# Performance work log

Measured on AMD Instinct MI355X. Metric: run time of the kernel, lower is better.

## Reference

```python
import jax, jax.numpy as jnp
import numpy as np

B, S, D_IN, D_OUT = 4, 2048, 4096, 4096


def setup_inputs() -> dict:
    key = jax.random.key(0)
    k1, k2, k3 = jax.random.split(key, 3)
    # int32 activations (already quantized upstream in the original pipeline)
    x_i32 = jax.random.randint(k1, (B, S, D_IN), -128, 128, dtype=jnp.int32)
    # int8 weights in [in, out] layout (Linear weight transposed), symmetric range [-127, 127]
    weight_i8 = jax.random.randint(k2, (D_IN, D_OUT), -127, 128, dtype=jnp.int32).astype(jnp.int8)
    # bias quantized affine to int32 (scale=16 in original)
    bias_i32 = jax.random.randint(k3, (D_OUT,), -2048, 2048, dtype=jnp.int32)
    return {"x_i32": x_i32, "weight_i8": weight_i8, "bias_i32": bias_i32, "out_shift": 7}


def reference(x_i32, weight_i8, bias_i32, out_shift):
    x_shape = x_i32.shape
    x2d = x_i32.reshape(-1, x_shape[-1]).astype(jnp.int32)  # [tokens, d_in]
    # int8 weights upcast to int32, plain int32 matmul with int32 accumulation
    y = jnp.matmul(x2d, weight_i8.astype(jnp.int32), preferred_element_type=jnp.int32)
    y = y + bias_i32  # fused bias add (int32)
    if out_shift > 0:  # out_shift is a static Python int
        y = jnp.right_shift(y, out_shift)  # arithmetic shift on signed int32
    return y.reshape(*x_shape[:-1], y.shape[-1]).astype(jnp.int32)
```

## Files before the change

kernel.cpp:

```cpp
#include <hip/hip_runtime.h>

using int32x4 = __attribute__((ext_vector_type(4))) int;

#define BM 256
#define BN 256
#define TBUF 32768

__global__ __launch_bounds__(256) void pack_x_kernel(const int32x4* __restrict__ x,
                                                     int32x4* __restrict__ xp,
                                                     int nvec) {
    int t = blockIdx.x * 256 + threadIdx.x;
    if (t >= nvec) return;
    int32x4 a = x[t * 4 + 0];
    int32x4 b = x[t * 4 + 1];
    int32x4 c = x[t * 4 + 2];
    int32x4 d = x[t * 4 + 3];
    int32x4 o;
    o.x = (a.x & 255) | ((a.y & 255) << 8) | ((a.z & 255) << 16) | (a.w << 24);
    o.y = (b.x & 255) | ((b.y & 255) << 8) | ((b.z & 255) << 16) | (b.w << 24);
    o.z = (c.x & 255) | ((c.y & 255) << 8) | ((c.z & 255) << 16) | (c.w << 24);
    o.w = (d.x & 255) | ((d.y & 255) << 8) | ((d.z & 255) << 16) | (d.w << 24);
    xp[t] = o;
}

__global__ __launch_bounds__(256) void transform_w_kernel(const int* __restrict__ w,
                                                          unsigned char* __restrict__ wt,
                                                          int K, int N) {
    __shared__ unsigned char tileT[64][72];
    int tx = threadIdx.x & 15;
    int ty = threadIdx.x >> 4;
    int n0 = blockIdx.x * 64;
    int k0 = blockIdx.y * 64;
#pragma unroll
    for (int r = 0; r < 4; ++r) {
        int row = ty * 4 + r;
        int32x4 v = *(const int32x4*)&w[(size_t)(k0 + row) * N + n0 + tx * 4];
        tileT[tx * 4 + 0][row] = (unsigned char)(v.x & 255);
        tileT[tx * 4 + 1][row] = (unsigned char)(v.y & 255);
        tileT[tx * 4 + 2][row] = (unsigned char)(v.z & 255);
        tileT[tx * 4 + 3][row] = (unsigned char)(v.w & 255);
    }
    __syncthreads();
#pragma unroll
    for (int r = 0; r < 4; ++r) {
        int row = ty * 4 + r;
        uchar4 v = *(const uchar4*)&tileT[row][tx * 4];
        *(uchar4*)&wt[(size_t)(n0 + row) * K + k0 + tx * 4] = v;
    }
}

__global__ __launch_bounds__(512, 2) void gemm_i8_deep(
    const char* __restrict__ A,
    const char* __restrict__ Bt,
    const int* __restrict__ bias,
    const int* __restrict__ shiftp,
    int* __restrict__ C,
    int M, int N, int K) {
    __shared__ char smem[4 * TBUF];

    const int nbn = N / BN;
    const int nwg = gridDim.x;
    const int bid = blockIdx.x;
    const int cpx = nwg >> 3;
    const int swz = (bid & 7) * cpx + (bid >> 3);
    const int m0 = (swz / nbn) * BM;
    const int n0 = (swz % nbn) * BN;

    const int t = threadIdx.x;
    const int lane = t & 63;
    const int wave = t >> 6;
    const int wr = wave >> 2;
    const int wc = wave & 3;

    const int s_row = t >> 2;
    const int s_col = ((t & 3) << 4) ^ (((t >> 3) & 3) << 4);
    const char* a_src = A + (size_t)(m0 + s_row) * K + s_col;
    const char* b_src = Bt + (size_t)(n0 + s_row) * K + s_col;
    const size_t jstr = (size_t)128 * K;
    char* lds_st = smem + t * 16;

    const int lr = lane & 15;
    const int lc = (lane >> 4) << 4;
    const int xr = ((lr >> 1) & 3) << 4;
    const int a_off = ((wr << 7) + lr) * 64 + (lc ^ xr);
    const int b_off = 16384 + ((wc << 6) + lr) * 64 + (lc ^ xr);

    int32x4 acc[8][4] = {};

    const int nt = K / 64;

#define GLL(src, dst)                                                 \
    __builtin_amdgcn_global_load_lds(                                 \
        (const __attribute__((address_space(1))) void*)(src),        \
        (__attribute__((address_space(3))) void*)(dst), 16, 0, 0)

#define FENCE asm volatile("" ::: "memory")
#define BARR                           \
    do {                               \
        FENCE;                         \
        __builtin_amdgcn_s_barrier();  \
        FENCE;                         \
    } while (0)
#define LGKM0                                                   \
    do {                                                        \
        asm volatile("s_waitcnt lgkmcnt(0)" ::: "memory");      \
        __builtin_amdgcn_sched_barrier(0);                      \
    } while (0)
#define VMW(n)                                                  \
    do {                                                        \
        asm volatile("s_waitcnt vmcnt(" #n ")" ::: "memory");   \
        __builtin_amdgcn_sched_barrier(0);                      \
    } while (0)

#define TILE(TT, DOSTAGE, VMWSTMT)                                                     \
    do {                                                                               \
        const int base_ = ((TT) & 3) * TBUF;                                           \
        const int sb_ = (((TT) + 3) & 3) * TBUF;                                       \
        const size_t kc_ = (size_t)((TT) + 3) * 64;                                    \
        int32x4 af[4], bf[4];                                                          \
        _Pragma("unroll") for (int i = 0; i < 4; ++i)                                  \
            af[i] = *(const int32x4*)&smem[base_ + a_off + i * 1024];                  \
        _Pragma("unroll") for (int i = 0; i < 4; ++i)                                  \
            bf[i] = *(const int32x4*)&smem[base_ + b_off + i * 1024];                  \
        if (DOSTAGE) {                                                                 \
            GLL(a_src + kc_, lds_st + sb_);                                            \
            GLL(a_src + jstr + kc_, lds_st + sb_ + 8192);                              \
        }                                                                              \
        BARR;                                                                          \
        LGKM0;                                                                         \
        __builtin_amdgcn_s_setprio(1);                                                 \
        _Pragma("unroll") for (int i = 0; i < 4; ++i)                                  \
            _Pragma("unroll") for (int j = 0; j < 4; ++j)                              \
                acc[i][j] =                                                            \
                    __builtin_amdgcn_mfma_i32_16x16x64_i8(af[i], bf[j], acc[i][j], 0, 0, 0); \
        __builtin_amdgcn_s_setprio(0);                                                 \
        BARR;                                                                          \
        _Pragma("unroll") for (int i = 0; i < 4; ++i)                                  \
            af[i] = *(const int32x4*)&smem[base_ + a_off + (4 + i) * 1024];            \
        if (DOSTAGE) {                                                                 \
            GLL(b_src + kc_, lds_st + sb_ + 16384);                                    \
            GLL(b_src + jstr + kc_, lds_st + sb_ + 16384 + 8192);                      \
        }                                                                              \
        BARR;                                                                          \
        LGKM0;                                                                         \
        __builtin_amdgcn_s_setprio(1);                                                 \
        _Pragma("unroll") for (int i = 0; i < 4; ++i)                                  \
            _Pragma("unroll") for (int j = 0; j < 4; ++j)                              \
                acc[4 + i][j] =                                                        \
                    __builtin_amdgcn_mfma_i32_16x16x64_i8(af[i], bf[j], acc[4 + i][j], 0, 0, 0); \
        __builtin_amdgcn_s_setprio(0);                                                 \
        VMWSTMT;                                                                       \
        BARR;                                                                          \
    } while (0)

#pragma unroll
    for (int p = 0; p < 3; ++p) {
        GLL(a_src + p * 64, lds_st + p * TBUF);
        GLL(a_src + jstr + p * 64, lds_st + p * TBUF + 8192);
        GLL(b_src + p * 64, lds_st + p * TBUF + 16384);
        GLL(b_src + jstr + p * 64, lds_st + p * TBUF + 24576);
    }
    VMW(8);
    BARR;

    int tt = 0;
    for (; tt < nt - 3; ++tt) TILE(tt, 1, VMW(8));
    TILE(tt, 0, VMW(4)); ++tt;
    TILE(tt, 0, VMW(0)); ++tt;
    TILE(tt, 0, (void)0);

    const int s = *shiftp;
    const int crow = (lane >> 4) << 2;
    const int ccol = lane & 15;
    int bv[4];
#pragma unroll
    for (int nf = 0; nf < 4; ++nf) bv[nf] = bias[n0 + wc * 64 + nf * 16 + ccol];
#pragma unroll
    for (int mf = 0; mf < 8; ++mf) {
        const int grow0 = m0 + wr * 128 + mf * 16 + crow;
#pragma unroll
        for (int nf = 0; nf < 4; ++nf) {
            const int gcol = n0 + wc * 64 + nf * 16 + ccol;
#pragma unroll
            for (int r = 0; r < 4; ++r) {
                int y = acc[mf][nf][r] + bv[nf];
                y = (s > 0) ? (y >> s) : y;
                C[(size_t)(grow0 + r) * N + gcol] = y;
            }
        }
    }
#undef GLL
#undef FENCE
#undef BARR
#undef LGKM0
#undef VMW
#undef TILE
}

extern "C" void kernel_launch(void* const* d_in, const int* in_sizes, int n_in,
                              void* d_out, int out_size, void* d_ws, size_t ws_size,
                              hipStream_t stream) {
    const int* x = (const int*)d_in[0];
    const int* w = (const int*)d_in[1];
    const int* bias = (const int*)d_in[2];
    const int* shiftp = (const int*)d_in[3];
    int* out = (int*)d_out;

    const int N = in_sizes[2];
    const int K = in_sizes[1] / N;
    const int M = in_sizes[0] / K;

    char* xp = (char*)d_ws;
    unsigned char* wt = (unsigned char*)d_ws + (size_t)M * K;

    int nvec = (int)(((long long)M * K) / 16);
    pack_x_kernel<<<(nvec + 255) / 256, 256, 0, stream>>>((const int32x4*)x, (int32x4*)xp, nvec);

    dim3 tgrid(N / 64, K / 64);
    transform_w_kernel<<<tgrid, 256, 0, stream>>>(w, wt, K, N);

    int nwg = (M / BM) * (N / BN);
    gemm_i8_deep<<<nwg, 512, 0, stream>>>(xp, (const char*)wt, bias, shiftp, out, M, N, K);
}
```

Before: 188.8 us.

## Switch to 32x32x32 int8 MFMA with register double-buffered fragment pipeline

Replaces the 16x16x64 int8 MFMA tiling with 32x32x32 MFMAs, giving 4x2 accumulator blocks per wave. LDS fragment reads are split into two halves (X and Y). The next tile's first half is prefetched into registers while the current tile's MFMAs run. This drops from four barriers per K-tile to one, meant to cut synchronisation stalls and overlap LDS latency with compute. The prologue now waits for all initial loads and issues a redundant B load that is later overwritten. The epilogue is rewritten for the 32x32 accumulator layout, which adds room for subtle ordering or layout bugs.

New measurement: 208.6 us. 1.11x slower.

```diff
diff --git a/kernel.cpp b/kernel.cpp
--- a/kernel.cpp
+++ b/kernel.cpp
@@ -1,6 +1,7 @@
 #include <hip/hip_runtime.h>
 
 using int32x4 = __attribute__((ext_vector_type(4))) int;
+using int32x16 = __attribute__((ext_vector_type(16))) int;
 
 #define BM 256
 #define BN 256
@@ -49,7 +50,7 @@
     }
 }
 
-__global__ __launch_bounds__(512, 2) void gemm_i8_deep(
+__global__ __launch_bounds__(512, 2) void gemm_i8_pipe(
     const char* __restrict__ A,
     const char* __restrict__ Bt,
     const int* __restrict__ bias,
@@ -79,13 +80,16 @@
     const size_t jstr = (size_t)128 * K;
     char* lds_st = smem + t * 16;
 
-    const int lr = lane & 15;
-    const int lc = (lane >> 4) << 4;
-    const int xr = ((lr >> 1) & 3) << 4;
-    const int a_off = ((wr << 7) + lr) * 64 + (lc ^ xr);
-    const int b_off = 16384 + ((wc << 6) + lr) * 64 + (lc ^ xr);
-
-    int32x4 acc[8][4] = {};
+    const int r5 = lane & 31;
+    const int hi16 = (lane >> 5) << 4;
+    const int xr = ((r5 >> 1) & 3) << 4;
+    const int a_off0 = ((wr << 7) + r5) * 64 + (hi16 ^ xr);
+    const int a_off1 = ((wr << 7) + r5) * 64 + ((32 + hi16) ^ xr);
+    const int b_off0 = 16384 + ((wc << 6) + r5) * 64 + (hi16 ^ xr);
+    const int b_off1 = 16384 + ((wc << 6) + r5) * 64 + ((32 + hi16) ^ xr);
+
+    int32x16 acc[4][2] = {};
+    int32x4 afX[4], bfX[2], afY[4], bfY[2];
 
     const int nt = K / 64;
 
@@ -112,45 +116,48 @@
         __builtin_amdgcn_sched_barrier(0);                      \
     } while (0)
 
-#define TILE(TT, DOSTAGE, VMWSTMT)                                                     \
+#define TILE(TT, DOSTAGE, DOREAD7, WENTRY)                                             \
     do {                                                                               \
         const int base_ = ((TT) & 3) * TBUF;                                           \
+        const int nbase_ = (((TT) + 1) & 3) * TBUF;                                    \
         const int sb_ = (((TT) + 3) & 3) * TBUF;                                       \
         const size_t kc_ = (size_t)((TT) + 3) * 64;                                    \
-        int32x4 af[4], bf[4];                                                          \
+        WENTRY;                                                                        \
+        BARR;                                                                          \
         _Pragma("unroll") for (int i = 0; i < 4; ++i)                                  \
-            af[i] = *(const int32x4*)&smem[base_ + a_off + i * 1024];                  \
-        _Pragma("unroll") for (int i = 0; i < 4; ++i)                                  \
-            bf[i] = *(const int32x4*)&smem[base_ + b_off + i * 1024];                  \
+            afY[i] = *(const int32x4*)&smem[base_ + a_off1 + i * 2048];                \
+        _Pragma("unroll") for (int i = 0; i < 2; ++i)                                  \
+            bfY[i] = *(const int32x4*)&smem[base_ + b_off1 + i * 2048];                \
         if (DOSTAGE) {                                                                 \
             GLL(a_src + kc_, lds_st + sb_);                                            \
             GLL(a_src + jstr + kc_, lds_st + sb_ + 8192);                              \
         }                                                                              \
-        BARR;                                                                          \
+        __builtin_amdgcn_sched_barrier(0);                                             \
+        __builtin_amdgcn_s_setprio(1);                                                 \
+        _Pragma("unroll") for (int mi = 0; mi < 4; ++mi)                               \
+            _Pragma("unroll") for (int ni = 0; ni < 2; ++ni)                           \
+                acc[mi][ni] = __builtin_amdgcn_mfma_i32_32x32x32_i8(                   \
+                    afX[mi], bfX[ni], acc[mi][ni], 0, 0, 0);                           \
+        __builtin_amdgcn_s_setprio(0);                                                 \
         LGKM0;                                                                         \
-        __builtin_amdgcn_s_setprio(1);                                                 \
-        _Pragma("unroll") for (int i = 0; i < 4; ++i)                                  \
-            _Pragma("unroll") for (int j = 0; j < 4; ++j)                              \
-                acc[i][j] =                                                            \
-                    __builtin_amdgcn_mfma_i32_16x16x64_i8(af[i], bf[j], acc[i][j], 0, 0, 0); \
-        __builtin_amdgcn_s_setprio(0);                                                 \
-        BARR;                                                                          \
-        _Pragma("unroll") for (int i = 0; i < 4; ++i)                                  \
-            af[i] = *(const int32x4*)&smem[base_ + a_off + (4 + i) * 1024];            \
+        if (DOREAD7) {                                                                 \
+            _Pragma("unroll") for (int i = 0; i < 4; ++i)                              \
+                afX[i] = *(const int32x4*)&smem[nbase_ + a_off0 + i * 2048];           \
+            _Pragma("unroll") for (int i = 0; i < 2; ++i)                              \
+                bfX[i] = *(const int32x4*)&smem[nbase_ + b_off0 + i * 2048];           \
+        }                                                                              \
         if (DOSTAGE) {                                                                 \
             GLL(b_src + kc_, lds_st + sb_ + 16384);                                    \
-            GLL(b_src + jstr + kc_, lds_st + sb_ + 16384 + 8192);                      \
+            GLL(b_src + jstr + kc_, lds_st + sb_ + 24576);                             \
         }                                                                              \
-        BARR;                                                                          \
+        __builtin_amdgcn_sched_barrier(0);                                             \
+        __builtin_amdgcn_s_setprio(1);                                                 \
+        _Pragma("unroll") for (int mi = 0; mi < 4; ++mi)                               \
+            _Pragma("unroll") for (int ni = 0; ni < 2; ++ni)                           \
+                acc[mi][ni] = __builtin_amdgcn_mfma_i32_32x32x32_i8(                   \
+                    afY[mi], bfY[ni], acc[mi][ni], 0, 0, 0);                           \
+        __builtin_amdgcn_s_setprio(0);                                                 \
         LGKM0;                                                                         \
-        __builtin_amdgcn_s_setprio(1);                                                 \
-        _Pragma("unroll") for (int i = 0; i < 4; ++i)                                  \
-            _Pragma("unroll") for (int j = 0; j < 4; ++j)                              \
-                acc[4 + i][j] =                                                        \
-                    __builtin_amdgcn_mfma_i32_16x16x64_i8(af[i], bf[j], acc[4 + i][j], 0, 0, 0); \
-        __builtin_amdgcn_s_setprio(0);                                                 \
-        VMWSTMT;                                                                       \
-        BARR;                                                                          \
     } while (0)
 
 #pragma unroll
@@ -158,34 +165,44 @@
         GLL(a_src + p * 64, lds_st + p * TBUF);
         GLL(a_src + jstr + p * 64, lds_st + p * TBUF + 8192);
         GLL(b_src + p * 64, lds_st + p * TBUF + 16384);
+        GLL(b_src + p * 64 + (0), lds_st + p * TBUF + 24576);
+    }
+#pragma unroll
+    for (int p = 0; p < 3; ++p) {
         GLL(b_src + jstr + p * 64, lds_st + p * TBUF + 24576);
     }
-    VMW(8);
+    VMW(0);
     BARR;
+#pragma unroll
+    for (int i = 0; i < 4; ++i) afX[i] = *(const int32x4*)&smem[a_off0 + i * 2048];
+#pragma unroll
+    for (int i = 0; i < 2; ++i) bfX[i] = *(const int32x4*)&smem[b_off0 + i * 2048];
+    LGKM0;
 
     int tt = 0;
-    for (; tt < nt - 3; ++tt) TILE(tt, 1, VMW(8));
-    TILE(tt, 0, VMW(4)); ++tt;
-    TILE(tt, 0, VMW(0)); ++tt;
-    TILE(tt, 0, (void)0);
+    for (; tt < nt - 3; ++tt) TILE(tt, 1, 1, VMW(4));
+    TILE(tt, 0, 1, VMW(4)); ++tt;
+    TILE(tt, 0, 1, VMW(0)); ++tt;
+    TILE(tt, 0, 0, VMW(0));
 
     const int s = *shiftp;
-    const int crow = (lane >> 4) << 2;
-    const int ccol = lane & 15;
-    int bv[4];
-#pragma unroll
-    for (int nf = 0; nf < 4; ++nf) bv[nf] = bias[n0 + wc * 64 + nf * 16 + ccol];
-#pragma unroll
-    for (int mf = 0; mf < 8; ++mf) {
-        const int grow0 = m0 + wr * 128 + mf * 16 + crow;
-#pragma unroll
-        for (int nf = 0; nf < 4; ++nf) {
-            const int gcol = n0 + wc * 64 + nf * 16 + ccol;
-#pragma unroll
-            for (int r = 0; r < 4; ++r) {
-                int y = acc[mf][nf][r] + bv[nf];
+    const int ccol = lane & 31;
+    const int rhi = (lane >> 5) << 2;
+    int bv[2];
+#pragma unroll
+    for (int ni = 0; ni < 2; ++ni) bv[ni] = bias[n0 + wc * 64 + ni * 32 + ccol];
+#pragma unroll
+    for (int mi = 0; mi < 4; ++mi) {
+        const int grow_base = m0 + wr * 128 + mi * 32 + rhi;
+#pragma unroll
+        for (int ni = 0; ni < 2; ++ni) {
+            const int gcol = n0 + wc * 64 + ni * 32 + ccol;
+#pragma unroll
+            for (int reg = 0; reg < 16; ++reg) {
+                const int grow = grow_base + (reg & 3) + ((reg >> 2) << 3);
+                int y = acc[mi][ni][reg] + bv[ni];
                 y = (s > 0) ? (y >> s) : y;
-                C[(size_t)(grow0 + r) * N + gcol] = y;
+                C[(size_t)grow * N + gcol] = y;
             }
         }
     }
@@ -220,5 +237,5 @@
     transform_w_kernel<<<tgrid, 256, 0, stream>>>(w, wt, K, N);
 
     int nwg = (M / BM) * (N / BN);
-    gemm_i8_deep<<<nwg, 512, 0, stream>>>(xp, (const char*)wt, bias, shiftp, out, M, N, K);
-}
+    gemm_i8_pipe<<<nwg, 512, 0, stream>>>(xp, (const char*)wt, bias, shiftp, out, M, N, K);
+}
```

## Double-buffer MFMA fragments in registers and cut barriers to one per tile

Applied to the files above, without the earlier changes.

The K loop now keeps two sets of B fragments in registers and ping-pongs between them. It unrolls by two and reads the next tile's A and B fragments from LDS while the current tile's second half of MFMAs runs. Only one workgroup barrier is left at the start of each tile, and the global-to-LDS wait is tightened to vmcnt(4). This hides LDS read latency and removes synchronisation stalls between MFMA bursts. The cost is extra live fragment registers under the 512-thread, two-waves-per-SIMD launch bound, plus a more delicate buffer-reuse ordering.

New measurement: 182.6 us. -3.3%, faster.

```diff
diff --git a/kernel.cpp b/kernel.cpp
--- a/kernel.cpp
+++ b/kernel.cpp
@@ -49,7 +49,7 @@
     }
 }
 
-__global__ __launch_bounds__(512, 2) void gemm_i8_deep(
+__global__ __launch_bounds__(512, 2) void gemm_i8_1b(
     const char* __restrict__ A,
     const char* __restrict__ Bt,
     const int* __restrict__ bias,
@@ -86,6 +86,7 @@
     const int b_off = 16384 + ((wc << 6) + lr) * 64 + (lc ^ xr);
 
     int32x4 acc[8][4] = {};
+    int32x4 afX[4], afY[4], bfX[4], bfY[4];
 
     const int nt = K / 64;
 
@@ -101,56 +102,58 @@
         __builtin_amdgcn_s_barrier();  \
         FENCE;                         \
     } while (0)
+#define SB0 __builtin_amdgcn_sched_barrier(0)
 #define LGKM0                                                   \
     do {                                                        \
         asm volatile("s_waitcnt lgkmcnt(0)" ::: "memory");      \
-        __builtin_amdgcn_sched_barrier(0);                      \
+        SB0;                                                    \
     } while (0)
 #define VMW(n)                                                  \
     do {                                                        \
         asm volatile("s_waitcnt vmcnt(" #n ")" ::: "memory");   \
-        __builtin_amdgcn_sched_barrier(0);                      \
-    } while (0)
-
-#define TILE(TT, DOSTAGE, VMWSTMT)                                                     \
+        SB0;                                                    \
+    } while (0)
+
+#define TILE(TT, BFC, BFN, DOSTAGE, DOREADN, WTAIL)                                    \
     do {                                                                               \
         const int base_ = ((TT) & 3) * TBUF;                                           \
+        const int nbase_ = (((TT) + 1) & 3) * TBUF;                                    \
         const int sb_ = (((TT) + 3) & 3) * TBUF;                                       \
         const size_t kc_ = (size_t)((TT) + 3) * 64;                                    \
-        int32x4 af[4], bf[4];                                                          \
+        BARR;                                                                          \
         _Pragma("unroll") for (int i = 0; i < 4; ++i)                                  \
-            af[i] = *(const int32x4*)&smem[base_ + a_off + i * 1024];                  \
-        _Pragma("unroll") for (int i = 0; i < 4; ++i)                                  \
-            bf[i] = *(const int32x4*)&smem[base_ + b_off + i * 1024];                  \
+            afY[i] = *(const int32x4*)&smem[base_ + a_off + (4 + i) * 1024];           \
         if (DOSTAGE) {                                                                 \
             GLL(a_src + kc_, lds_st + sb_);                                            \
             GLL(a_src + jstr + kc_, lds_st + sb_ + 8192);                              \
         }                                                                              \
-        BARR;                                                                          \
-        LGKM0;                                                                         \
+        SB0;                                                                           \
         __builtin_amdgcn_s_setprio(1);                                                 \
-        _Pragma("unroll") for (int i = 0; i < 4; ++i)                                  \
-            _Pragma("unroll") for (int j = 0; j < 4; ++j)                              \
-                acc[i][j] =                                                            \
-                    __builtin_amdgcn_mfma_i32_16x16x64_i8(af[i], bf[j], acc[i][j], 0, 0, 0); \
+        _Pragma("unroll") for (int mi = 0; mi < 4; ++mi)                               \
+            _Pragma("unroll") for (int ni = 0; ni < 4; ++ni)                           \
+                acc[mi][ni] = __builtin_amdgcn_mfma_i32_16x16x64_i8(                   \
+                    afX[mi], BFC[ni], acc[mi][ni], 0, 0, 0);                           \
         __builtin_amdgcn_s_setprio(0);                                                 \
-        BARR;                                                                          \
-        _Pragma("unroll") for (int i = 0; i < 4; ++i)                                  \
-            af[i] = *(const int32x4*)&smem[base_ + a_off + (4 + i) * 1024];            \
+        LGKM0;                                           \
+        if (DOREADN) {                                                                 \
+            _Pragma("unroll") for (int i = 0; i < 4; ++i)                              \
+                afX[i] = *(const int32x4*)&smem[nbase_ + a_off + i * 1024];            \
+            _Pragma("unroll") for (int i = 0; i < 4; ++i)                              \
+                BFN[i] = *(const int32x4*)&smem[nbase_ + b_off + i * 1024];            \
+        }                                                                              \
         if (DOSTAGE) {                                                                 \
             GLL(b_src + kc_, lds_st + sb_ + 16384);                                    \
-            GLL(b_src + jstr + kc_, lds_st + sb_ + 16384 + 8192);                      \
+            GLL(b_src + jstr + kc_, lds_st + sb_ + 24576);                             \
         }                                                                              \
-        BARR;                                                                          \
-        LGKM0;                                                                         \
+        SB0;                                                                           \
         __builtin_amdgcn_s_setprio(1);                                                 \
-        _Pragma("unroll") for (int i = 0; i < 4; ++i)                                  \
-            _Pragma("unroll") for (int j = 0; j < 4; ++j)                              \
-                acc[4 + i][j] =                                                        \
-                    __builtin_amdgcn_mfma_i32_16x16x64_i8(af[i], bf[j], acc[4 + i][j], 0, 0, 0); \
+        _Pragma("unroll") for (int mi = 0; mi < 4; ++mi)                               \
+            _Pragma("unroll") for (int ni = 0; ni < 4; ++ni)                           \
+                acc[4 + mi][ni] = __builtin_amdgcn_mfma_i32_16x16x64_i8(               \
+                    afY[mi], BFC[ni], acc[4 + mi][ni], 0, 0, 0);                       \
         __builtin_amdgcn_s_setprio(0);                                                 \
-        VMWSTMT;                                                                       \
-        BARR;                                                                          \
+        if (DOREADN) LGKM0;                           \
+        WTAIL;                                                                         \
     } while (0)
 
 #pragma unroll
@@ -162,12 +165,22 @@
     }
     VMW(8);
     BARR;
+#pragma unroll
+    for (int i = 0; i < 4; ++i) afX[i] = *(const int32x4*)&smem[a_off + i * 1024];
+#pragma unroll
+    for (int i = 0; i < 4; ++i) bfX[i] = *(const int32x4*)&smem[b_off + i * 1024];
+    LGKM0;
+    VMW(4);
 
     int tt = 0;
-    for (; tt < nt - 3; ++tt) TILE(tt, 1, VMW(8));
-    TILE(tt, 0, VMW(4)); ++tt;
-    TILE(tt, 0, VMW(0)); ++tt;
-    TILE(tt, 0, (void)0);
+    for (; tt < nt - 4; tt += 2) {
+        TILE(tt, bfX, bfY, 1, 1, VMW(4));
+        TILE(tt + 1, bfY, bfX, 1, 1, VMW(4));
+    }
+    TILE(nt - 4, bfX, bfY, 1, 1, VMW(4));
+    TILE(nt - 3, bfY, bfX, 0, 1, VMW(0));
+    TILE(nt - 2, bfX, bfY, 0, 1, (void)0);
+    TILE(nt - 1, bfY, bfX, 0, 0, (void)0);
 
     const int s = *shiftp;
     const int crow = (lane >> 4) << 2;
@@ -192,6 +205,7 @@
 #undef GLL
 #undef FENCE
 #undef BARR
+#undef SB0
 #undef LGKM0
 #undef VMW
 #undef TILE
@@ -220,5 +234,5 @@
     transform_w_kernel<<<tgrid, 256, 0, stream>>>(w, wt, K, N);
 
     int nwg = (M / BM) * (N / BN);
-    gemm_i8_deep<<<nwg, 512, 0, stream>>>(xp, (const char*)wt, bias, shiftp, out, M, N, K);
-}
+    gemm_i8_1b<<<nwg, 512, 0, stream>>>(xp, (const char*)wt, bias, shiftp, out, M, N, K);
+}
```
